# Kernel tuning notes

Hardware: AMD Instinct MI355X
Metric: run time of the kernel (lower is better)

## Reference

```python
import jax, jax.numpy as jnp
import numpy as np

D_MODEL = 768
NUM_HEADS = 12
DEPTH = D_MODEL // NUM_HEADS


def setup_inputs() -> dict:
    key = jax.random.key(0)
    ks = jax.random.split(key, 11)
    B, S, D = 2, 2048, D_MODEL
    scale = 1.0 / np.sqrt(D)
    inp = {
        "v": jax.random.normal(ks[0], (B, S, D), jnp.float32),
        "k": jax.random.normal(ks[1], (B, S, D), jnp.float32),
        "q": jax.random.normal(ks[2], (B, S, D), jnp.float32),
        "wq": jax.random.normal(ks[3], (D, D), jnp.float32) * scale,
        "bq": jnp.zeros((D,), jnp.float32),
        "wk": jax.random.normal(ks[4], (D, D), jnp.float32) * scale,
        "bk": jnp.zeros((D,), jnp.float32),
        "wv": jax.random.normal(ks[5], (D, D), jnp.float32) * scale,
        "bv": jnp.zeros((D,), jnp.float32),
        "wo": jax.random.normal(ks[6], (D, D), jnp.float32) * scale,
        "bo": jnp.zeros((D,), jnp.float32),
    }
    return inp


def _split_heads(x):
    # (B, S, D) -> (B, H, S, depth)
    B, S, _ = x.shape
    return x.reshape(B, S, NUM_HEADS, DEPTH).transpose(0, 2, 1, 3)


def reference(v, k, q, wq, bq, wk, bk, wv, bv, wo, bo):
    B, S, D = q.shape
    qh = _split_heads(q @ wq + bq)  # (B,H,S,dh)
    kh = _split_heads(k @ wk + bk)
    vh = _split_heads(v @ wv + bv)
    logits = jnp.einsum("bhqd,bhkd->bhqk", qh, kh) / jnp.sqrt(
        jnp.asarray(DEPTH, qh.dtype)
    )
    attn = jax.nn.softmax(logits, axis=-1)  # (B,H,S,S)
    ctx = jnp.einsum("bhqk,bhkd->bhqd", attn, vh)
    ctx = ctx.transpose(0, 2, 1, 3).reshape(B, S, D)
    return ctx @ wo + bo
```

## Files before the change

### kernel.cpp

```cpp
#include <hip/hip_runtime.h>
#include <hip/hip_bf16.h>
#include <math.h>

typedef __bf16 bf16;
typedef __attribute__((ext_vector_type(8))) __bf16 bf16x8;
typedef __attribute__((ext_vector_type(4))) __bf16 bf16x4v;
typedef __attribute__((ext_vector_type(4))) float f32x4;

#define MFMA16(a, b, c) __builtin_amdgcn_mfma_f32_16x16x32_bf16(a, b, c, 0, 0, 0)

__device__ __forceinline__ void gld16(const bf16* g, bf16* l) {
  __builtin_amdgcn_global_load_lds((const __attribute__((address_space(1))) void*)g,
                                   (__attribute__((address_space(3))) void*)l, 16, 0, 0);
}

__global__ __launch_bounds__(256) void prep(const float* __restrict__ q,
                                            const float* __restrict__ k,
                                            const float* __restrict__ v,
                                            bf16* __restrict__ qb, bf16* __restrict__ kb,
                                            bf16* __restrict__ vb,
                                            const float* __restrict__ w0,
                                            const float* __restrict__ w1,
                                            const float* __restrict__ w2,
                                            const float* __restrict__ w3,
                                            bf16* __restrict__ t0, bf16* __restrict__ t1,
                                            bf16* __restrict__ t2, bf16* __restrict__ t3) {
  const int lin = blockIdx.x;
  if (lin < 4608) {
    const int which = lin / 1536, idx = lin % 1536;
    const float* a = which == 0 ? q : (which == 1 ? k : v);
    bf16* o = which == 0 ? qb : (which == 1 ? kb : vb);
    const size_t i = ((size_t)idx * 256 + threadIdx.x) * 8;
    const float4 f0 = *(const float4*)(a + i);
    const float4 f1 = *(const float4*)(a + i + 4);
    bf16x8 r = {(bf16)f0.x, (bf16)f0.y, (bf16)f0.z, (bf16)f0.w,
                (bf16)f1.x, (bf16)f1.y, (bf16)f1.z, (bf16)f1.w};
    *(bf16x8*)(o + i) = r;
  } else {
    const int w = lin - 4608;
    const int z = w / 576, rem = w % 576;
    const int by = rem / 24, bx = rem % 24;
    const float* W = z == 0 ? w0 : (z == 1 ? w1 : (z == 2 ? w2 : w3));
    bf16* T = z == 0 ? t0 : (z == 1 ? t1 : (z == 2 ? t2 : t3));
    __shared__ float t[32][33];
    const int tx = threadIdx.x & 31, ty = threadIdx.x >> 5;
    const int c0 = bx * 32, r0 = by * 32;
#pragma unroll
    for (int i = 0; i < 4; ++i) {
      const int r = ty + 8 * i;
      t[r][tx] = W[(size_t)(r0 + r) * 768 + c0 + tx];
    }
    __syncthreads();
#pragma unroll
    for (int i = 0; i < 4; ++i) {
      const int r = ty + 8 * i;
      T[(size_t)(c0 + r) * 768 + r0 + tx] = (bf16)t[tx][r];
    }
  }
}

__device__ __forceinline__ void gemm_core(const bf16* __restrict__ A, const bf16* __restrict__ BT,
                                          int row0, int col0, bf16* As, bf16* Bs,
                                          f32x4 acc[4][4]) {
  const int tid = threadIdx.x;
  const int lane = tid & 63, wave = tid >> 6;
  const int m15 = lane & 15, kg = lane >> 4;
  const int wm = wave >> 1, wn = wave & 1;
  const int pr16 = lane & 15;
  const int pk8 = (lane >> 4) * 8;
#pragma unroll
  for (int i = 0; i < 4; ++i)
#pragma unroll
    for (int j = 0; j < 4; ++j) acc[i][j] = f32x4{0.f, 0.f, 0.f, 0.f};

  for (int k0 = 0; k0 < 768; k0 += 32) {
#pragma unroll
    for (int j = 0; j < 2; ++j) {
      const int i = wave * 2 + j;
      gld16(A + (size_t)(row0 + 16 * i + pr16) * 768 + k0 + pk8, As + i * 512);
      gld16(BT + (size_t)(col0 + 16 * i + pr16) * 768 + k0 + pk8, Bs + i * 512);
    }
    __syncthreads();
    bf16x8 af[4], bfr[4];
#pragma unroll
    for (int t = 0; t < 4; ++t)
      af[t] = *(const bf16x8*)(As + (4 * wm + t) * 512 + kg * 128 + m15 * 8);
#pragma unroll
    for (int t = 0; t < 4; ++t)
      bfr[t] = *(const bf16x8*)(Bs + (4 * wn + t) * 512 + kg * 128 + m15 * 8);
#pragma unroll
    for (int mt = 0; mt < 4; ++mt)
#pragma unroll
      for (int nt = 0; nt < 4; ++nt) acc[mt][nt] = MFMA16(af[mt], bfr[nt], acc[mt][nt]);
    __syncthreads();
  }
}

__global__ __launch_bounds__(256, 3) void gemm_qkv(
    const bf16* __restrict__ qb, const bf16* __restrict__ kb, const bf16* __restrict__ vb,
    const bf16* __restrict__ wqT, const bf16* __restrict__ wkT, const bf16* __restrict__ wvT,
    const float* __restrict__ bq, const float* __restrict__ bk, const float* __restrict__ bv,
    bf16* __restrict__ Qh, bf16* __restrict__ Kh, bf16* __restrict__ Vt) {
  __shared__ bf16 As[128 * 32], Bs[128 * 32];
  const bf16 *A, *BT;
  const float* bias;
  bf16* out;
  int mode;
  if (blockIdx.z == 0) { A = qb; BT = wqT; bias = bq; out = Qh; mode = 0; }
  else if (blockIdx.z == 1) { A = kb; BT = wkT; bias = bk; out = Kh; mode = 0; }
  else { A = vb; BT = wvT; bias = bv; out = Vt; mode = 1; }
  const int row0 = blockIdx.y * 128, col0 = blockIdx.x * 128;
  f32x4 acc[4][4];
  gemm_core(A, BT, row0, col0, As, Bs, acc);

  const int lane = threadIdx.x & 63, wave = threadIdx.x >> 6;
  const int m15 = lane & 15, kg = lane >> 4;
  const int wm = wave >> 1, wn = wave & 1;
#pragma unroll
  for (int mt = 0; mt < 4; ++mt) {
#pragma unroll
    for (int nt = 0; nt < 4; ++nt) {
      const int col = col0 + 64 * wn + 16 * nt + m15;
      const float bb = bias[col];
      const int h = col >> 6, d = col & 63;
      const int rowb = row0 + 64 * wm + 16 * mt + kg * 4;
      const int b = rowb >> 11, s0 = rowb & 2047;
      if (mode == 0) {
#pragma unroll
        for (int r = 0; r < 4; ++r)
          out[((size_t)(b * 12 + h) * 2048 + s0 + r) * 64 + d] = (bf16)(acc[mt][nt][r] + bb);
      } else {
        bf16x4v pk;
#pragma unroll
        for (int r = 0; r < 4; ++r) pk[r] = (bf16)(acc[mt][nt][r] + bb);
        *(bf16x4v*)&out[((size_t)(b * 12 + h) * 64 + d) * 2048 + s0] = pk;
      }
    }
  }
}

__global__ __launch_bounds__(256, 3) void gemm_out(const bf16* __restrict__ A,
                                                   const bf16* __restrict__ BT,
                                                   const float* __restrict__ bias,
                                                   float* __restrict__ out) {
  __shared__ bf16 As[64 * 32], Bs[64 * 32];
  const int tid = threadIdx.x;
  const int lane = tid & 63, wave = tid >> 6;
  const int m15 = lane & 15, kg = lane >> 4;
  const int wm = wave >> 1, wn = wave & 1;
  const int row0 = blockIdx.y * 64, col0 = blockIdx.x * 64;
  const int pr16 = lane & 15, pk8 = (lane >> 4) * 8;

  f32x4 acc[2][2];
#pragma unroll
  for (int i = 0; i < 2; ++i)
#pragma unroll
    for (int j = 0; j < 2; ++j) acc[i][j] = f32x4{0.f, 0.f, 0.f, 0.f};

  for (int k0 = 0; k0 < 768; k0 += 32) {
    gld16(A + (size_t)(row0 + 16 * wave + pr16) * 768 + k0 + pk8, As + wave * 512);
    gld16(BT + (size_t)(col0 + 16 * wave + pr16) * 768 + k0 + pk8, Bs + wave * 512);
    __syncthreads();
    bf16x8 af[2], bfr[2];
#pragma unroll
    for (int t = 0; t < 2; ++t)
      af[t] = *(const bf16x8*)(As + (2 * wm + t) * 512 + kg * 128 + m15 * 8);
#pragma unroll
    for (int t = 0; t < 2; ++t)
      bfr[t] = *(const bf16x8*)(Bs + (2 * wn + t) * 512 + kg * 128 + m15 * 8);
#pragma unroll
    for (int mt = 0; mt < 2; ++mt)
#pragma unroll
      for (int nt = 0; nt < 2; ++nt) acc[mt][nt] = MFMA16(af[mt], bfr[nt], acc[mt][nt]);
    __syncthreads();
  }
#pragma unroll
  for (int mt = 0; mt < 2; ++mt) {
#pragma unroll
    for (int nt = 0; nt < 2; ++nt) {
      const int col = col0 + 32 * wn + 16 * nt + m15;
      const float bb = bias[col];
#pragma unroll
      for (int r = 0; r < 4; ++r) {
        const int row = row0 + 32 * wm + 16 * mt + kg * 4 + r;
        out[(size_t)row * 768 + col] = acc[mt][nt][r] + bb;
      }
    }
  }
}

__global__ __launch_bounds__(256, 3) void attn_kernel(const bf16* __restrict__ Q,
                                                      const bf16* __restrict__ K,
                                                      const bf16* __restrict__ VT,
                                                      bf16* __restrict__ ctx) {
  __shared__ __align__(16) char SMEM[33792];

  const int tid = threadIdx.x;
  const int lane = tid & 63, wave = tid >> 6;
  const int m15 = lane & 15, kg = lane >> 4;
  const int lin = blockIdx.x;
  const int bh = lin % 24, rg = lin / 24;
  const size_t hb = (size_t)bh * 2048 * 64;
  const bf16* Qp = Q + hb;
  const bf16* Kp = K + hb;
  const bf16* Vp = VT + hb;
  const int qrow0 = rg * 64;
  bf16* Pw = (bf16*)SMEM + wave * 2560;

  bf16x8 qf[4][2];
#pragma unroll
  for (int rt = 0; rt < 4; ++rt)
#pragma unroll
    for (int ks = 0; ks < 2; ++ks) {
      bf16x8 tv = *(const bf16x8*)&Qp[(size_t)(qrow0 + 16 * rt + m15) * 64 + 32 * ks + kg * 8];
#pragma unroll
      for (int j = 0; j < 8; ++j) tv[j] = (bf16)((float)tv[j] * 0.125f);
      qf[rt][ks] = tv;
    }

  f32x4 o[4][4];
  float lp[4];
#pragma unroll
  for (int rt = 0; rt < 4; ++rt) {
#pragma unroll
    for (int mt = 0; mt < 4; ++mt) o[rt][mt] = f32x4{0.f, 0.f, 0.f, 0.f};
    lp[rt] = 0.f;
  }

  const int kbase = wave * 512;
  for (int c = 0; c < 16; ++c) {
    const int kc = kbase + c * 32;
    bf16x8 kf[2][2];
#pragma unroll
    for (int kt = 0; kt < 2; ++kt)
#pragma unroll
      for (int ks = 0; ks < 2; ++ks)
        kf[kt][ks] = *(const bf16x8*)&Kp[(size_t)(kc + 16 * kt + m15) * 64 + 32 * ks + kg * 8];
    bf16x8 vf[4];
#pragma unroll
    for (int mt = 0; mt < 4; ++mt)
      vf[mt] = *(const bf16x8*)&Vp[(size_t)(16 * mt + m15) * 2048 + kc + kg * 8];
    f32x4 s[2][4];
#pragma unroll
    for (int kt = 0; kt < 2; ++kt)
#pragma unroll
      for (int rt = 0; rt < 4; ++rt) s[kt][rt] = f32x4{0.f, 0.f, 0.f, 0.f};
#pragma unroll
    for (int ks = 0; ks < 2; ++ks)
#pragma unroll
      for (int kt = 0; kt < 2; ++kt)
#pragma unroll
        for (int rt = 0; rt < 4; ++rt) s[kt][rt] = MFMA16(kf[kt][ks], qf[rt][ks], s[kt][rt]);
#pragma unroll
    for (int kt = 0; kt < 2; ++kt)
#pragma unroll
      for (int rt = 0; rt < 4; ++rt) {
        bf16x4v pk;
#pragma unroll
        for (int r = 0; r < 4; ++r) {
          const float pe = __expf(s[kt][rt][r]);
          lp[rt] += pe;
          pk[r] = (bf16)pe;
        }
        *(bf16x4v*)&Pw[rt * 640 + m15 * 40 + 16 * kt + 4 * kg] = pk;
      }
    asm volatile("s_waitcnt lgkmcnt(0)" ::: "memory");
#pragma unroll
    for (int rt = 0; rt < 4; ++rt) {
      const bf16x8 pf = *(const bf16x8*)&Pw[rt * 640 + m15 * 40 + kg * 8];
#pragma unroll
      for (int mt = 0; mt < 4; ++mt) o[rt][mt] = MFMA16(vf[mt], pf, o[rt][mt]);
    }
  }

#pragma unroll
  for (int rt = 0; rt < 4; ++rt) {
    lp[rt] += __shfl_xor(lp[rt], 16);
    lp[rt] += __shfl_xor(lp[rt], 32);
  }

  float* R0 = (float*)SMEM;
  float* R1 = (float*)(SMEM + 16384);
  float* LP = (float*)(SMEM + 32768);
  __syncthreads();
  if (kg == 0) {
#pragma unroll
    for (int rt = 0; rt < 4; ++rt) LP[wave * 64 + rt * 16 + m15] = lp[rt];
  }
  if (wave == 1 || wave == 3) {
    float* R = (wave == 1) ? R0 : R1;
#pragma unroll
    for (int rt = 0; rt < 4; ++rt)
#pragma unroll
      for (int mt = 0; mt < 4; ++mt)
        *(f32x4*)&R[((rt * 4 + mt) * 64 + lane) * 4] = o[rt][mt];
  }
  __syncthreads();
  if (wave == 0 || wave == 2) {
    float* R = (wave == 0) ? R0 : R1;
#pragma unroll
    for (int rt = 0; rt < 4; ++rt)
#pragma unroll
      for (int mt = 0; mt < 4; ++mt) {
        const f32x4 po = *(const f32x4*)&R[((rt * 4 + mt) * 64 + lane) * 4];
#pragma unroll
        for (int j = 0; j < 4; ++j) o[rt][mt][j] += po[j];
      }
  }
  __syncthreads();
  if (wave == 2) {
#pragma unroll
    for (int rt = 0; rt < 4; ++rt)
#pragma unroll
      for (int mt = 0; mt < 4; ++mt)
        *(f32x4*)&R1[((rt * 4 + mt) * 64 + lane) * 4] = o[rt][mt];
  }
  __syncthreads();
  if (wave == 0) {
    const int b = bh / 12, h = bh % 12;
#pragma unroll
    for (int rt = 0; rt < 4; ++rt) {
      const float lsum = LP[0 * 64 + rt * 16 + m15] + LP[1 * 64 + rt * 16 + m15] +
                         LP[2 * 64 + rt * 16 + m15] + LP[3 * 64 + rt * 16 + m15];
      const float inv = 1.0f / lsum;
      const int sr = qrow0 + 16 * rt + m15;
#pragma unroll
      for (int mt = 0; mt < 4; ++mt) {
        const f32x4 po = *(const f32x4*)&R1[((rt * 4 + mt) * 64 + lane) * 4];
        bf16x4v pk;
#pragma unroll
        for (int r = 0; r < 4; ++r) pk[r] = (bf16)((o[rt][mt][r] + po[r]) * inv);
        *(bf16x4v*)&ctx[((size_t)(b * 2048) + sr) * 768 + h * 64 + 16 * mt + 4 * kg] = pk;
      }
    }
  }
}

extern "C" void kernel_launch(void* const* d_in, const int* in_sizes, int n_in,
                              void* d_out, int out_size, void* d_ws, size_t ws_size,
                              hipStream_t stream) {
  const float* v = (const float*)d_in[0];
  const float* k = (const float*)d_in[1];
  const float* q = (const float*)d_in[2];
  const float* wq = (const float*)d_in[3];
  const float* bq = (const float*)d_in[4];
  const float* wk = (const float*)d_in[5];
  const float* bk = (const float*)d_in[6];
  const float* wv = (const float*)d_in[7];
  const float* bv = (const float*)d_in[8];
  const float* wo = (const float*)d_in[9];
  const float* bo = (const float*)d_in[10];

  char* ws = (char*)d_ws;
  const size_t SEG = (size_t)4096 * 768 * sizeof(bf16);
  const size_t WSEG = (size_t)768 * 768 * sizeof(bf16);
  bf16* Qh = (bf16*)(ws + 0 * SEG);
  bf16* Kh = (bf16*)(ws + 1 * SEG);
  bf16* Vt = (bf16*)(ws + 2 * SEG);
  bf16* qb = (bf16*)(ws + 3 * SEG);
  bf16* kb = (bf16*)(ws + 4 * SEG);
  bf16* vb = (bf16*)(ws + 5 * SEG);
  bf16* ctx = qb;
  bf16* wqT = (bf16*)(ws + 6 * SEG);
  bf16* wkT = (bf16*)(ws + 6 * SEG + WSEG);
  bf16* wvT = (bf16*)(ws + 6 * SEG + 2 * WSEG);
  bf16* woT = (bf16*)(ws + 6 * SEG + 3 * WSEG);

  prep<<<dim3(6912), 256, 0, stream>>>(q, k, v, qb, kb, vb, wq, wk, wv, wo,
                                       wqT, wkT, wvT, woT);
  gemm_qkv<<<dim3(6, 32, 3), 256, 0, stream>>>(qb, kb, vb, wqT, wkT, wvT, bq, bk, bv,
                                               Qh, Kh, Vt);
  attn_kernel<<<dim3(768), 256, 0, stream>>>(Qh, Kh, Vt, ctx);
  gemm_out<<<dim3(12, 64), 256, 0, stream>>>(ctx, woT, bo, (float*)d_out);
}
```

Before: 217.9 us.

## Keep P in registers via f16 MFMA and retile QKV GEMM to 128x96

In the attention kernel, probabilities are converted to fp16 and fed straight into a 16x16x16 f16 MFMA with V stored as fp16. The score tile's output register layout matches the B operand layout, so the LDS round trip and the wait on P are no longer needed. The QKV projection now uses 128x96 tiles with a 8x32x3 grid, which raises the block count and changes how waves share the loads. Trade-offs: the MFMA has half the K depth, so more instructions are issued, and P and V lose some range by being held in fp16.

```diff
diff --git a/kernel.cpp b/kernel.cpp
--- a/kernel.cpp
+++ b/kernel.cpp
@@ -3,11 +3,14 @@
 #include <math.h>
 
 typedef __bf16 bf16;
+typedef _Float16 f16;
 typedef __attribute__((ext_vector_type(8))) __bf16 bf16x8;
 typedef __attribute__((ext_vector_type(4))) __bf16 bf16x4v;
+typedef __attribute__((ext_vector_type(4))) _Float16 half4;
 typedef __attribute__((ext_vector_type(4))) float f32x4;
 
 #define MFMA16(a, b, c) __builtin_amdgcn_mfma_f32_16x16x32_bf16(a, b, c, 0, 0, 0)
+#define MFMA16F16(a, b, c) __builtin_amdgcn_mfma_f32_16x16x16f16(a, b, c, 0, 0, 0)
 
 __device__ __forceinline__ void gld16(const bf16* g, bf16* l) {
   __builtin_amdgcn_global_load_lds((const __attribute__((address_space(1))) void*)g,
@@ -59,81 +62,77 @@
   }
 }
 
-__device__ __forceinline__ void gemm_core(const bf16* __restrict__ A, const bf16* __restrict__ BT,
-                                          int row0, int col0, bf16* As, bf16* Bs,
-                                          f32x4 acc[4][4]) {
+__global__ __launch_bounds__(256, 3) void gemm_qkv(
+    const bf16* __restrict__ qb, const bf16* __restrict__ kb, const bf16* __restrict__ vb,
+    const bf16* __restrict__ wqT, const bf16* __restrict__ wkT, const bf16* __restrict__ wvT,
+    const float* __restrict__ bq, const float* __restrict__ bk, const float* __restrict__ bv,
+    bf16* __restrict__ Qh, bf16* __restrict__ Kh, f16* __restrict__ Vt) {
+  __shared__ bf16 As[128 * 32];
+  __shared__ bf16 Bs[96 * 32];
+  const bf16 *A, *BT;
+  const float* bias;
+  int mode;
+  if (blockIdx.z == 0) { A = qb; BT = wqT; bias = bq; mode = 0; }
+  else if (blockIdx.z == 1) { A = kb; BT = wkT; bias = bk; mode = 0; }
+  else { A = vb; BT = wvT; bias = bv; mode = 1; }
+  const int row0 = blockIdx.y * 128, col0 = blockIdx.x * 96;
+
   const int tid = threadIdx.x;
   const int lane = tid & 63, wave = tid >> 6;
   const int m15 = lane & 15, kg = lane >> 4;
   const int wm = wave >> 1, wn = wave & 1;
-  const int pr16 = lane & 15;
-  const int pk8 = (lane >> 4) * 8;
+  const int pr16 = lane & 15, pk8 = (lane >> 4) * 8;
+
+  f32x4 acc[4][3];
 #pragma unroll
   for (int i = 0; i < 4; ++i)
 #pragma unroll
-    for (int j = 0; j < 4; ++j) acc[i][j] = f32x4{0.f, 0.f, 0.f, 0.f};
+    for (int j = 0; j < 3; ++j) acc[i][j] = f32x4{0.f, 0.f, 0.f, 0.f};
 
   for (int k0 = 0; k0 < 768; k0 += 32) {
 #pragma unroll
-    for (int j = 0; j < 2; ++j) {
-      const int i = wave * 2 + j;
-      gld16(A + (size_t)(row0 + 16 * i + pr16) * 768 + k0 + pk8, As + i * 512);
-      gld16(BT + (size_t)(col0 + 16 * i + pr16) * 768 + k0 + pk8, Bs + i * 512);
-    }
-    __syncthreads();
-    bf16x8 af[4], bfr[4];
+    for (int j = 0; j < 4; ++j) {
+      const int idx = wave * 4 + j;
+      if (idx < 8)
+        gld16(A + (size_t)(row0 + 16 * idx + pr16) * 768 + k0 + pk8, As + idx * 512);
+      else if (idx < 14)
+        gld16(BT + (size_t)(col0 + 16 * (idx - 8) + pr16) * 768 + k0 + pk8,
+              Bs + (idx - 8) * 512);
+    }
+    __syncthreads();
+    bf16x8 af[4], bfr[3];
 #pragma unroll
     for (int t = 0; t < 4; ++t)
       af[t] = *(const bf16x8*)(As + (4 * wm + t) * 512 + kg * 128 + m15 * 8);
 #pragma unroll
-    for (int t = 0; t < 4; ++t)
-      bfr[t] = *(const bf16x8*)(Bs + (4 * wn + t) * 512 + kg * 128 + m15 * 8);
+    for (int t = 0; t < 3; ++t)
+      bfr[t] = *(const bf16x8*)(Bs + (3 * wn + t) * 512 + kg * 128 + m15 * 8);
 #pragma unroll
     for (int mt = 0; mt < 4; ++mt)
 #pragma unroll
-      for (int nt = 0; nt < 4; ++nt) acc[mt][nt] = MFMA16(af[mt], bfr[nt], acc[mt][nt]);
-    __syncthreads();
-  }
-}
-
-__global__ __launch_bounds__(256, 3) void gemm_qkv(
-    const bf16* __restrict__ qb, const bf16* __restrict__ kb, const bf16* __restrict__ vb,
-    const bf16* __restrict__ wqT, const bf16* __restrict__ wkT, const bf16* __restrict__ wvT,
-    const float* __restrict__ bq, const float* __restrict__ bk, const float* __restrict__ bv,
-    bf16* __restrict__ Qh, bf16* __restrict__ Kh, bf16* __restrict__ Vt) {
-  __shared__ bf16 As[128 * 32], Bs[128 * 32];
-  const bf16 *A, *BT;
-  const float* bias;
-  bf16* out;
-  int mode;
-  if (blockIdx.z == 0) { A = qb; BT = wqT; bias = bq; out = Qh; mode = 0; }
-  else if (blockIdx.z == 1) { A = kb; BT = wkT; bias = bk; out = Kh; mode = 0; }
-  else { A = vb; BT = wvT; bias = bv; out = Vt; mode = 1; }
-  const int row0 = blockIdx.y * 128, col0 = blockIdx.x * 128;
-  f32x4 acc[4][4];
-  gemm_core(A, BT, row0, col0, As, Bs, acc);
-
-  const int lane = threadIdx.x & 63, wave = threadIdx.x >> 6;
-  const int m15 = lane & 15, kg = lane >> 4;
-  const int wm = wave >> 1, wn = wave & 1;
+      for (int nt = 0; nt < 3; ++nt) acc[mt][nt] = MFMA16(af[mt], bfr[nt], acc[mt][nt]);
+    __syncthreads();
+  }
+
 #pragma unroll
   for (int mt = 0; mt < 4; ++mt) {
 #pragma unroll
-    for (int nt = 0; nt < 4; ++nt) {
-      const int col = col0 + 64 * wn + 16 * nt + m15;
+    for (int nt = 0; nt < 3; ++nt) {
+      const int col = col0 + 48 * wn + 16 * nt + m15;
       const float bb = bias[col];
       const int h = col >> 6, d = col & 63;
       const int rowb = row0 + 64 * wm + 16 * mt + kg * 4;
       const int b = rowb >> 11, s0 = rowb & 2047;
       if (mode == 0) {
+        bf16* out = (blockIdx.z == 0) ? Qh : Kh;
 #pragma unroll
         for (int r = 0; r < 4; ++r)
           out[((size_t)(b * 12 + h) * 2048 + s0 + r) * 64 + d] = (bf16)(acc[mt][nt][r] + bb);
       } else {
-        bf16x4v pk;
-#pragma unroll
-        for (int r = 0; r < 4; ++r) pk[r] = (bf16)(acc[mt][nt][r] + bb);
-        *(bf16x4v*)&out[((size_t)(b * 12 + h) * 64 + d) * 2048 + s0] = pk;
+        half4 pk;
+#pragma unroll
+        for (int r = 0; r < 4; ++r) pk[r] = (f16)(acc[mt][nt][r] + bb);
+        *(half4*)&Vt[((size_t)(b * 12 + h) * 64 + d) * 2048 + s0] = pk;
       }
     }
   }
@@ -191,7 +190,7 @@
 
 __global__ __launch_bounds__(256, 3) void attn_kernel(const bf16* __restrict__ Q,
                                                       const bf16* __restrict__ K,
-                                                      const bf16* __restrict__ VT,
+                                                      const f16* __restrict__ VT,
                                                       bf16* __restrict__ ctx) {
   __shared__ __align__(16) char SMEM[33792];
 
@@ -203,9 +202,8 @@
   const size_t hb = (size_t)bh * 2048 * 64;
   const bf16* Qp = Q + hb;
   const bf16* Kp = K + hb;
-  const bf16* Vp = VT + hb;
+  const f16* Vp = VT + hb;
   const int qrow0 = rg * 64;
-  bf16* Pw = (bf16*)SMEM + wave * 2560;
 
   bf16x8 qf[4][2];
 #pragma unroll
@@ -236,40 +234,35 @@
 #pragma unroll
       for (int ks = 0; ks < 2; ++ks)
         kf[kt][ks] = *(const bf16x8*)&Kp[(size_t)(kc + 16 * kt + m15) * 64 + 32 * ks + kg * 8];
-    bf16x8 vf[4];
-#pragma unroll
-    for (int mt = 0; mt < 4; ++mt)
-      vf[mt] = *(const bf16x8*)&Vp[(size_t)(16 * mt + m15) * 2048 + kc + kg * 8];
-    f32x4 s[2][4];
+    half4 vf[2][4];
 #pragma unroll
     for (int kt = 0; kt < 2; ++kt)
 #pragma unroll
-      for (int rt = 0; rt < 4; ++rt) s[kt][rt] = f32x4{0.f, 0.f, 0.f, 0.f};
-#pragma unroll
-    for (int ks = 0; ks < 2; ++ks)
-#pragma unroll
-      for (int kt = 0; kt < 2; ++kt)
-#pragma unroll
-        for (int rt = 0; rt < 4; ++rt) s[kt][rt] = MFMA16(kf[kt][ks], qf[rt][ks], s[kt][rt]);
-#pragma unroll
-    for (int kt = 0; kt < 2; ++kt)
+      for (int mt = 0; mt < 4; ++mt)
+        vf[kt][mt] = *(const half4*)&Vp[(size_t)(16 * mt + m15) * 2048 + kc + 16 * kt + 4 * kg];
+
+#pragma unroll
+    for (int kt = 0; kt < 2; ++kt) {
+      f32x4 s[4];
+#pragma unroll
+      for (int rt = 0; rt < 4; ++rt) s[rt] = f32x4{0.f, 0.f, 0.f, 0.f};
+#pragma unroll
+      for (int ks = 0; ks < 2; ++ks)
+#pragma unroll
+        for (int rt = 0; rt < 4; ++rt) s[rt] = MFMA16(kf[kt][ks], qf[rt][ks], s[rt]);
 #pragma unroll
       for (int rt = 0; rt < 4; ++rt) {
-        bf16x4v pk;
+        half4 p;
 #pragma unroll
         for (int r = 0; r < 4; ++r) {
-          const float pe = __expf(s[kt][rt][r]);
+          const float pe = __expf(s[rt][r]);
           lp[rt] += pe;
-          pk[r] = (bf16)pe;
+          p[r] = (f16)pe;
         }
-        *(bf16x4v*)&Pw[rt * 640 + m15 * 40 + 16 * kt + 4 * kg] = pk;
-      }
-    asm volatile("s_waitcnt lgkmcnt(0)" ::: "memory");
-#pragma unroll
-    for (int rt = 0; rt < 4; ++rt) {
-      const bf16x8 pf = *(const bf16x8*)&Pw[rt * 640 + m15 * 40 + kg * 8];
-#pragma unroll
-      for (int mt = 0; mt < 4; ++mt) o[rt][mt] = MFMA16(vf[mt], pf, o[rt][mt]);
+#pragma unroll
+        for (int mt = 0; mt < 4; ++mt)
+          o[rt][mt] = MFMA16F16(vf[kt][mt], p, o[rt][mt]);
+      }
     }
   }
 
@@ -356,7 +349,7 @@
   const size_t WSEG = (size_t)768 * 768 * sizeof(bf16);
   bf16* Qh = (bf16*)(ws + 0 * SEG);
   bf16* Kh = (bf16*)(ws + 1 * SEG);
-  bf16* Vt = (bf16*)(ws + 2 * SEG);
+  f16* Vt = (f16*)(ws + 2 * SEG);
   bf16* qb = (bf16*)(ws + 3 * SEG);
   bf16* kb = (bf16*)(ws + 4 * SEG);
   bf16* vb = (bf16*)(ws + 5 * SEG);
@@ -368,7 +361,7 @@
 
   prep<<<dim3(6912), 256, 0, stream>>>(q, k, v, qb, kb, vb, wq, wk, wv, wo,
                                        wqT, wkT, wvT, woT);
-  gemm_qkv<<<dim3(6, 32, 3), 256, 0, stream>>>(qb, kb, vb, wqT, wkT, wvT, bq, bk, bv,
+  gemm_qkv<<<dim3(8, 32, 3), 256, 0, stream>>>(qb, kb, vb, wqT, wkT, wvT, bq, bk, bv,
                                                Qh, Kh, Vt);
   attn_kernel<<<dim3(768), 256, 0, stream>>>(Qh, Kh, Vt, ctx);
   gemm_out<<<dim3(12, 64), 256, 0, stream>>>(ctx, woT, bo, (float*)d_out);
```

Measured after the change: 233.4 us. +7.1%, slower.
